# Kernel optimization log

Measured on AMD Instinct MI355X. Metric: run time of the kernel, lower is better.

The kernel has to match this reference:

```python
import jax, jax.numpy as jnp
import numpy as np

B, T, M, H, P, C = 1024, 100, 128, 128, 128, 32  # batch, time, sensors, enc_hid, dec_hid, classes


def setup_inputs() -> dict:
    key = jax.random.key(0)
    ks = jax.random.split(key, 20)
    def n(k, shape, s=0.05):
        return jax.random.normal(k, shape, dtype=jnp.float32) * s
    return {
        "X": n(ks[0], (B, T, M), 1.0),
        # encoder LSTM (input_size=M, hidden=H), PyTorch gate order i,f,g,o
        "enc_Wih": n(ks[1], (4 * H, M)),
        "enc_Whh": n(ks[2], (4 * H, H)),
        "enc_bih": n(ks[3], (4 * H,)),
        "enc_bhh": n(ks[4], (4 * H,)),
        # encoder attention Linear(2H+T -> 1)
        "enc_attn_W": n(ks[5], (1, 2 * H + T)),
        "enc_attn_b": n(ks[6], (1,)),
        # decoder attn: Linear(2P+H -> H), Tanh, Linear(H -> 1)
        "dec_W1": n(ks[7], (H, 2 * P + H)),
        "dec_b1": n(ks[8], (H,)),
        "dec_W2": n(ks[9], (1, H)),
        "dec_b2": n(ks[10], (1,)),
        # decoder LSTM (input_size=1, hidden=P)
        "dec_Wih": n(ks[11], (4 * P, 1)),
        "dec_Whh": n(ks[12], (4 * P, P)),
        "dec_bih": n(ks[13], (4 * P,)),
        "dec_bhh": n(ks[14], (4 * P,)),
        # fc: Linear(H -> 1) with weight.data.normal_() (std 1)
        "fc_W": n(ks[15], (1, H), 1.0),
        "fc_b": n(ks[16], (1,)),
        # fc_final: Linear(P+H -> num_class)
        "fcf_W": n(ks[17], (C, P + H)),
        "fcf_b": n(ks[18], (C,)),
    }


def _lstm_step(x, h, c, Wih, Whh, bih, bhh):
    g = x @ Wih.T + bih + h @ Whh.T + bhh
    i, f, gg, o = jnp.split(g, 4, axis=-1)
    c = jax.nn.sigmoid(f) * c + jax.nn.sigmoid(i) * jnp.tanh(gg)
    h = jax.nn.sigmoid(o) * jnp.tanh(c)
    return h, c


def reference(X, enc_Wih, enc_Whh, enc_bih, enc_bhh, enc_attn_W, enc_attn_b,
              dec_W1, dec_b1, dec_W2, dec_b2,
              dec_Wih, dec_Whh, dec_bih, dec_bhh,
              fc_W, fc_b, fcf_W, fcf_b):
    Bn = X.shape[0]
    XT = jnp.swapaxes(X, 1, 2)  # [B, M, T] constant across encoder steps
    h0 = jnp.zeros((Bn, H), X.dtype)

    def enc_step(carry, x_t):  # x_t: [B, M]
        h, c = carry
        z = jnp.concatenate([
            jnp.broadcast_to(h[:, None, :], (Bn, M, H)),
            jnp.broadcast_to(c[:, None, :], (Bn, M, H)),
            XT,
        ], axis=-1)  # [B, M, 2H+T]
        score = jnp.einsum('bmf,f->bm', z, enc_attn_W[0]) + enc_attn_b[0]
        alpha = jax.nn.softmax(score, axis=1)
        x_tilde = alpha * x_t
        h, c = _lstm_step(x_tilde, h, c, enc_Wih, enc_Whh, enc_bih, enc_bhh)
        return (h, c), h

    _, hs = jax.lax.scan(enc_step, (h0, h0), jnp.swapaxes(X, 0, 1))
    X_enc = jnp.swapaxes(hs, 0, 1)  # [B, T, H]

    d0 = jnp.zeros((Bn, P), X.dtype)
    ctx0 = jnp.zeros((Bn, H), X.dtype)

    def dec_step(carry, _):
        d, c, _ctx = carry
        z = jnp.concatenate([
            jnp.broadcast_to(d[:, None, :], (Bn, T, P)),
            jnp.broadcast_to(c[:, None, :], (Bn, T, P)),
            X_enc,
        ], axis=-1)  # [B, T, 2P+H]
        hid = jnp.tanh(jnp.einsum('btf,hf->bth', z, dec_W1) + dec_b1)
        score = jnp.einsum('bth,h->bt', hid, dec_W2[0]) + dec_b2[0]
        beta = jax.nn.softmax(score, axis=1)
        ctx = jnp.einsum('bt,bth->bh', beta, X_enc)  # [B, H]
        y_tilde = ctx @ fc_W.T + fc_b  # [B, 1]
        d, c = _lstm_step(y_tilde, d, c, dec_Wih, dec_Whh, dec_bih, dec_bhh)
        return (d, c, ctx), None

    (d, c, ctx), _ = jax.lax.scan(dec_step, (d0, d0, ctx0), None, length=T)
    return jnp.concatenate([d, ctx], axis=-1) @ fcf_W.T + fcf_b  # [B, num_class]
```

## Files before the change

kernel.cpp:

```cpp
#include <hip/hip_runtime.h>


typedef unsigned int   u32;
typedef unsigned short u16;

#define T_  100
#define C_  32
#define NT  512
#define BPB 4
#define TS  132
#define QS  (T_ * NT)
#define SP  160

typedef __attribute__((ext_vector_type(2))) __fp16 h16x2;
typedef __attribute__((ext_vector_type(8))) __fp16 h16x8;
typedef __attribute__((ext_vector_type(4))) float  f32x4;

#if __has_builtin(__builtin_amdgcn_fdot2)
#define HAVE_FDOT2 1
#else
#define HAVE_FDOT2 0
#endif

__device__ __forceinline__ u32 pkh2(float a, float b) {
#if __has_builtin(__builtin_amdgcn_cvt_pkrtz)
  h16x2 p = __builtin_amdgcn_cvt_pkrtz(a, b);
  return __builtin_bit_cast(u32, p);
#else
  union { __fp16 h[2]; u32 u; } v;
  v.h[0] = (__fp16)a; v.h[1] = (__fp16)b;
  return v.u;
#endif
}
__device__ __forceinline__ void unph(u32 p, float& lo, float& hi) {
  union { u32 u; __fp16 h[2]; } v; v.u = p;
  lo = (float)v.h[0]; hi = (float)v.h[1];
}
__device__ __forceinline__ u16 f2h(float f) {
  union { __fp16 h; u16 u; } v; v.h = (__fp16)f; return v.u;
}
__device__ __forceinline__ float h2f(u16 u) {
  union { u16 u; __fp16 h; } v; v.u = u; return (float)v.h;
}
__device__ __forceinline__ float dot2h(u32 w, u32 x, float acc) {
#if HAVE_FDOT2
  return __builtin_amdgcn_fdot2(__builtin_bit_cast(h16x2, w),
                                __builtin_bit_cast(h16x2, x),
                                acc, false);
#else
  float a, b, c, d;
  unph(w, a, b); unph(x, c, d);
  return fmaf(a, c, fmaf(b, d, acc));
#endif
}
__device__ __forceinline__ h16x8 pack8(const float* p) {
  float4 v0 = *(const float4*)p;
  float4 v1 = *(const float4*)(p + 4);
  uint4 u;
  u.x = pkh2(v0.x, v0.y); u.y = pkh2(v0.z, v0.w);
  u.z = pkh2(v1.x, v1.y); u.w = pkh2(v1.z, v1.w);
  return __builtin_bit_cast(h16x8, u);
}
__device__ __forceinline__ h16x8 ldb(const u16* p, int off) {
  return __builtin_bit_cast(h16x8, *(const uint4*)(p + off));
}

#if __has_builtin(__builtin_amdgcn_rcpf)
__device__ __forceinline__ float rcpf_(float x){ return __builtin_amdgcn_rcpf(x); }
#else
__device__ __forceinline__ float rcpf_(float x){ return 1.0f / x; }
#endif
__device__ __forceinline__ float sigm(float x){ return rcpf_(1.0f + __expf(-x)); }
__device__ __forceinline__ float tanh_(float x){
  return 1.0f - 2.0f * rcpf_(1.0f + __expf(2.0f * x));
}
__device__ __forceinline__ u32 tanhpk(u32 eu, u32 uu) {
  h16x2 x = __builtin_bit_cast(h16x2, eu) + __builtin_bit_cast(h16x2, uu);
  const h16x2 one  = {(__fp16)1.0f,  (__fp16)1.0f};
#if __has_builtin(__builtin_elementwise_max) && __has_builtin(__builtin_elementwise_min)
  const h16x2 mone = {(__fp16)-1.0f, (__fp16)-1.0f};
  x = __builtin_elementwise_min(one, __builtin_elementwise_max(x, mone));
#else
  {
    float lo, hi; unph(__builtin_bit_cast(u32, x), lo, hi);
    x = (h16x2){(__fp16)fminf(1.f, fmaxf(-1.f, lo)),
                (__fp16)fminf(1.f, fmaxf(-1.f, hi))};
  }
#endif
  h16x2 x2 = x * x;
  const h16x2 c1 = {(__fp16)0.1333333f,  (__fp16)0.1333333f};
  const h16x2 c0 = {(__fp16)-0.3333333f, (__fp16)-0.3333333f};
  h16x2 r = x * (x2 * (x2 * c1 + c0) + one);
  return __builtin_bit_cast(u32, r);
}
__device__ __forceinline__ float ptanh(float x){
  x = fminf(1.0f, fmaxf(-1.0f, x));
  float x2 = x * x;
  float p  = fmaf(x2, 0.1333333f, -0.3333333f);
  return x * fmaf(x2, p, 1.0f);
}
__device__ __forceinline__ float wsum(float v){
  #pragma unroll
  for (int o = 32; o; o >>= 1) v += __shfl_xor(v, o, 64);
  return v;
}

__global__ void __launch_bounds__(NT)
darnn4(const float* __restrict__ X,
       const float* __restrict__ eWih, const float* __restrict__ eWhh,
       const float* __restrict__ ebih, const float* __restrict__ ebhh,
       const float* __restrict__ eAw,  const float* __restrict__ eAb,
       const float* __restrict__ dW1,  const float* __restrict__ db1,
       const float* __restrict__ dW2,  const float* __restrict__ db2,
       const float* __restrict__ dWih, const float* __restrict__ dWhh,
       const float* __restrict__ dbih, const float* __restrict__ dbhh,
       const float* __restrict__ fcW,  const float* __restrict__ fcb,
       const float* __restrict__ fcfW, const float* __restrict__ fcfb,
       u16* __restrict__ qws,
       float* __restrict__ out)
{
  __shared__ __align__(16) u16   sE1[BPB][T_ * TS];
  __shared__ __align__(16) float sg[BPB][520];
  __shared__ __align__(16) float sh[BPB][128];
  __shared__ __align__(16) float sc[BPB][128];
  __shared__ __align__(16) u16   shp[BPB][SP];
  __shared__ __align__(16) u16   scp[BPB][SP];
  __shared__ __align__(16) float su[BPB][128];
  __shared__ __align__(16) float spart[BPB][512];
  __shared__ __align__(16) float sye[BPB][128];
  __shared__ __align__(16) u32   su2[BPB][68];
  __shared__ __align__(16) u32   sw2p[64];
  __shared__ float sred[16];

  const int tid  = threadIdx.x;
  const int lane = tid & 63;
  const int wv   = tid >> 6;
  const int hh   = tid & 127;
  const int q4   = tid >> 7;
  const int nn   = lane & 15;
  const int kg   = lane >> 4;
  const bool wr  = (nn < BPB);
  const int b0   = blockIdx.x * BPB;

  (void)eAb; (void)db2;

  if (tid < 64) sw2p[tid] = pkh2(dW2[2 * tid], dW2[2 * tid + 1]);

  {
    const float* xp = X + (size_t)(b0 + q4) * 12800 + hh;
    float sval = 0.f;
    #pragma unroll 4
    for (int t = 0; t < T_; ++t) sval += xp[t * 128] * eAw[256 + t];
    float e = __expf(sval);
    float s = wsum(e);
    if (lane == 0) sred[wv] = s;
    __syncthreads();
    float al = e * rcpf_(sred[q4 * 2] + sred[q4 * 2 + 1]);
    #pragma unroll 4
    for (int t = 0; t < T_; ++t)
      sE1[q4][t * TS + hh] = f2h(al * xp[t * 128]);
    sh[q4][hh] = 0.f; sc[q4][hh] = 0.f; shp[q4][hh] = 0; scp[q4][hh] = 0;
  }
  __syncthreads();

  {
    u32 wq[64];
    const float4* wi = (const float4*)(eWih + (size_t)tid * 128);
    #pragma unroll
    for (int i = 0; i < 32; ++i) {
      float4 v = wi[i];
      wq[2*i]   = pkh2(v.x, v.y);
      wq[2*i+1] = pkh2(v.z, v.w);
    }
    #pragma unroll 1
    for (int bg = 0; bg < BPB; ++bg) {
      u16* qb = qws + (size_t)(b0 + bg) * QS;
      #pragma unroll 1
      for (int t = 0; t < T_; ++t) {
        const uint2* xr = (const uint2*)(&sE1[bg][t * TS]);
        float a0 = 0.f, a1 = 0.f;
        #pragma unroll
        for (int k = 0; k < 16; ++k) {
          uint2 xv = xr[k];
          a0 = dot2h(wq[2*k],   xv.x, a0);
          a1 = dot2h(wq[2*k+1], xv.y, a1);
        }
        qb[t * NT + tid] = f2h(a0 + a1);
      }
    }
  }
  __syncthreads();

  {
    h16x8 aH[16];
    #pragma unroll
    for (int rt = 0; rt < 4; ++rt)
      #pragma unroll
      for (int ks = 0; ks < 4; ++ks)
        aH[rt*4+ks] = pack8(eWhh + (size_t)(wv*64 + rt*16 + nn) * 128
                            + ks*32 + kg*8);
    float bgx = ebih[hh]       + ebhh[hh];
    float bgy = ebih[hh + 128] + ebhh[hh + 128];
    float bgz = ebih[hh + 256] + ebhh[hh + 256];
    float bgw = ebih[hh + 384] + ebhh[hh + 384];
    const u16* qrow = qws + (size_t)(b0 + q4) * QS + hh;

    for (int t = 0; t < T_; ++t) {
      u16 qv0 = qrow[t * NT];
      u16 qv1 = qrow[t * NT + 128];
      u16 qv2 = qrow[t * NT + 256];
      u16 qv3 = qrow[t * NT + 384];
      f32x4 g0 = {0,0,0,0}, g1 = {0,0,0,0}, g2 = {0,0,0,0}, g3 = {0,0,0,0};
      #pragma unroll
      for (int ks = 0; ks < 4; ++ks) {
        h16x8 b = ldb(&shp[nn & 3][0], ks*32 + kg*8);
        g0 = __builtin_amdgcn_mfma_f32_16x16x32_f16(aH[0*4+ks], b, g0, 0,0,0);
        g1 = __builtin_amdgcn_mfma_f32_16x16x32_f16(aH[1*4+ks], b, g1, 0,0,0);
        g2 = __builtin_amdgcn_mfma_f32_16x16x32_f16(aH[2*4+ks], b, g2, 0,0,0);
        g3 = __builtin_amdgcn_mfma_f32_16x16x32_f16(aH[3*4+ks], b, g3, 0,0,0);
      }
      if (wr) {
        *(f32x4*)(&sg[nn][wv*64 +  0 + kg*4]) = g0;
        *(f32x4*)(&sg[nn][wv*64 + 16 + kg*4]) = g1;
        *(f32x4*)(&sg[nn][wv*64 + 32 + kg*4]) = g2;
        *(f32x4*)(&sg[nn][wv*64 + 48 + kg*4]) = g3;
      }
      __syncthreads();
      {
        float gi = sigm (sg[q4][hh]       + bgx + h2f(qv0));
        float gf = sigm (sg[q4][hh + 128] + bgy + h2f(qv1));
        float gg = tanh_(sg[q4][hh + 256] + bgz + h2f(qv2));
        float go = sigm (sg[q4][hh + 384] + bgw + h2f(qv3));
        float c  = gf * sc[q4][hh] + gi * gg;
        sc[q4][hh] = c;
        float h  = go * tanh_(c);
        sh[q4][hh] = h;
        u16 hb = f2h(h);
        shp[q4][hh] = hb;
        scp[q4][hh] = f2h(c);
        qws[(size_t)(b0 + q4) * QS + t * NT + hh] = hb;
      }
      __syncthreads();
    }
  }

  if (hh < T_) {
    #pragma unroll 1
    for (int bg = 0; bg < BPB; ++bg) {
      const uint2* xe = (const uint2*)(qws + (size_t)(b0 + bg) * QS
                                       + hh * NT + q4 * 32);
      const float* fw = fcW + q4 * 32;
      float a = 0.f;
      #pragma unroll
      for (int k = 0; k < 8; ++k) {
        uint2 xv = xe[k];
        float l0, l1, l2, l3;
        unph(xv.x, l0, l1); unph(xv.y, l2, l3);
        a += fw[4*k]*l0 + fw[4*k+1]*l1 + fw[4*k+2]*l2 + fw[4*k+3]*l3;
      }
      spart[bg][hh * 4 + q4] = a;
    }
  }
  __syncthreads();
  if (hh < T_) {
    float4 p = ((const float4*)spart[q4])[hh];
    sye[q4][hh] = (p.x + p.y) + (p.z + p.w);
  }
  __syncthreads();

  {
    u32 wtp[64];
    const float4* w4p = (const float4*)(dW1 + (size_t)hh * 384 + 256);
    #pragma unroll
    for (int i = 0; i < 32; ++i) {
      float4 v = w4p[i];
      wtp[2*i]   = pkh2(v.x, v.y);
      wtp[2*i+1] = pkh2(v.z, v.w);
    }
    float b1v = db1[hh];
    #pragma unroll 1
    for (int bg = 0; bg < BPB; ++bg) {
      #pragma unroll 1
      for (int i = 0; i < 25; ++i) {
        int t = q4 * 25 + i;
        const uint2* xe = (const uint2*)(qws + (size_t)(b0 + bg) * QS + t * NT);
        float a0 = 0.f, a1 = 0.f;
        #pragma unroll
        for (int k = 0; k < 16; ++k) {
          uint2 xv = xe[k];
          a0 = dot2h(wtp[2*k],   xv.x, a0);
          a1 = dot2h(wtp[2*k+1], xv.y, a1);
        }
        sE1[bg][t * TS + hh] = f2h(a0 + a1 + b1v);
      }
    }
  }

  h16x8 aD[16];
  #pragma unroll
  for (int rt = 0; rt < 4; ++rt)
    #pragma unroll
    for (int ks = 0; ks < 4; ++ks)
      aD[rt*4+ks] = pack8(dWhh + (size_t)(wv*64 + rt*16 + nn) * 128
                          + ks*32 + kg*8);
  h16x8 aU[8];
  #pragma unroll
  for (int ks = 0; ks < 8; ++ks)
    aU[ks] = pack8(dW1 + (size_t)(wv*16 + nn) * 384 + ks*32 + kg*8);
  float bdx = dbih[hh]       + dbhh[hh];
  float bdy = dbih[hh + 128] + dbhh[hh + 128];
  float bdz = dbih[hh + 256] + dbhh[hh + 256];
  float bdw = dbih[hh + 384] + dbhh[hh + 384];
  float wix = dWih[hh];
  float wiy = dWih[hh + 128];
  float wiz = dWih[hh + 256];
  float wiw = dWih[hh + 384];
  float fcbv = fcb[0];
  sh[q4][hh] = 0.f; sc[q4][hh] = 0.f; shp[q4][hh] = 0; scp[q4][hh] = 0;
  __syncthreads();

  for (int step = 0; step < T_; ++step) {
    {
      f32x4 au = {0,0,0,0};
      #pragma unroll
      for (int ks = 0; ks < 8; ++ks) {
        const u16* bp = (ks < 4) ? &shp[nn & 3][0] : &scp[nn & 3][0];
        h16x8 b = ldb(bp, (ks & 3)*32 + kg*8);
        au = __builtin_amdgcn_mfma_f32_16x16x32_f16(aU[ks], b, au, 0,0,0);
      }
      if (wr) {
        uint2 up;
        up.x = pkh2(au[0], au[1]);
        up.y = pkh2(au[2], au[3]);
        *(uint2*)(&su2[nn][wv*8 + kg*2]) = up;
      }
    }
    {
      f32x4 g0 = {0,0,0,0}, g1 = {0,0,0,0}, g2 = {0,0,0,0}, g3 = {0,0,0,0};
      #pragma unroll
      for (int ks = 0; ks < 4; ++ks) {
        h16x8 b = ldb(&shp[nn & 3][0], ks*32 + kg*8);
        g0 = __builtin_amdgcn_mfma_f32_16x16x32_f16(aD[0*4+ks], b, g0, 0,0,0);
        g1 = __builtin_amdgcn_mfma_f32_16x16x32_f16(aD[1*4+ks], b, g1, 0,0,0);
        g2 = __builtin_amdgcn_mfma_f32_16x16x32_f16(aD[2*4+ks], b, g2, 0,0,0);
        g3 = __builtin_amdgcn_mfma_f32_16x16x32_f16(aD[3*4+ks], b, g3, 0,0,0);
      }
      if (wr) {
        *(f32x4*)(&sg[nn][wv*64 +  0 + kg*4]) = g0;
        *(f32x4*)(&sg[nn][wv*64 + 16 + kg*4]) = g1;
        *(f32x4*)(&sg[nn][wv*64 + 32 + kg*4]) = g2;
        *(f32x4*)(&sg[nn][wv*64 + 48 + kg*4]) = g3;
      }
    }
    __syncthreads();
    if (hh < T_) {
      const uint2* wp  = (const uint2*)(sw2p + q4 * 16);
      const uint2* e0p = (const uint2*)(&sE1[0][hh * TS + q4 * 32]);
      const uint2* e1p = (const uint2*)(&sE1[1][hh * TS + q4 * 32]);
      const uint2* e2p = (const uint2*)(&sE1[2][hh * TS + q4 * 32]);
      const uint2* e3p = (const uint2*)(&sE1[3][hh * TS + q4 * 32]);
      const uint2* u0p = (const uint2*)(su2[0] + q4 * 16);
      const uint2* u1p = (const uint2*)(su2[1] + q4 * 16);
      const uint2* u2p = (const uint2*)(su2[2] + q4 * 16);
      const uint2* u3p = (const uint2*)(su2[3] + q4 * 16);
      float ac0 = 0.f, ac1 = 0.f, ac2 = 0.f, ac3 = 0.f;
      #pragma unroll
      for (int j = 0; j < 8; ++j) {
        uint2 w2v = wp[j];
        uint2 ev, uv;
        ev = e0p[j]; uv = u0p[j];
        ac0 = dot2h(w2v.x, tanhpk(ev.x, uv.x), ac0);
        ac0 = dot2h(w2v.y, tanhpk(ev.y, uv.y), ac0);
        ev = e1p[j]; uv = u1p[j];
        ac1 = dot2h(w2v.x, tanhpk(ev.x, uv.x), ac1);
        ac1 = dot2h(w2v.y, tanhpk(ev.y, uv.y), ac1);
        ev = e2p[j]; uv = u2p[j];
        ac2 = dot2h(w2v.x, tanhpk(ev.x, uv.x), ac2);
        ac2 = dot2h(w2v.y, tanhpk(ev.y, uv.y), ac2);
        ev = e3p[j]; uv = u3p[j];
        ac3 = dot2h(w2v.x, tanhpk(ev.x, uv.x), ac3);
        ac3 = dot2h(w2v.y, tanhpk(ev.y, uv.y), ac3);
      }
      spart[0][hh * 4 + q4] = ac0;
      spart[1][hh * 4 + q4] = ac1;
      spart[2][hh * 4 + q4] = ac2;
      spart[3][hh * 4 + q4] = ac3;
    }
    __syncthreads();
    {
      float yv;
      {
        const int bg = q4;
        float4 p0 = ((const float4*)spart[bg])[lane];
        float e0 = __expf((p0.x + p0.y) + (p0.z + p0.w));
        float es = e0, ys = e0 * sye[bg][lane];
        if (lane < 36) {
          float4 p1 = ((const float4*)spart[bg])[64 + lane];
          float e1 = __expf((p1.x + p1.y) + (p1.z + p1.w));
          es += e1; ys += e1 * sye[bg][64 + lane];
        }
        es = wsum(es); ys = wsum(ys);
        yv = ys * rcpf_(es) + fcbv;
      }
      float gi = sigm (sg[q4][hh]       + bdx + wix * yv);
      float gf = sigm (sg[q4][hh + 128] + bdy + wiy * yv);
      float gg = tanh_(sg[q4][hh + 256] + bdz + wiz * yv);
      float go = sigm (sg[q4][hh + 384] + bdw + wiw * yv);
      float c  = gf * sc[q4][hh] + gi * gg;
      sc[q4][hh] = c;
      float d  = go * tanh_(c);
      sh[q4][hh] = d;
      shp[q4][hh] = f2h(d);
      scp[q4][hh] = f2h(c);
    }
    __syncthreads();
  }

  if (wv < BPB) {
    int bg = wv;
    float4 p0 = ((const float4*)spart[bg])[lane];
    float e0 = __expf((p0.x + p0.y) + (p0.z + p0.w));
    float e1 = 0.f;
    if (lane < 36) {
      float4 p1 = ((const float4*)spart[bg])[64 + lane];
      e1 = __expf((p1.x + p1.y) + (p1.z + p1.w));
    }
    float iv = rcpf_(wsum(e0 + e1));
    sye[bg][lane] = e0 * iv;
    if (lane < 36) sye[bg][64 + lane] = e1 * iv;
  }
  __syncthreads();
  {
    const u16* xeb = qws + (size_t)(b0 + q4) * QS + hh;
    float cx = 0.f;
    #pragma unroll 4
    for (int t = 0; t < T_; ++t)
      cx += sye[q4][t] * h2f(xeb[t * NT]);
    su[q4][hh] = cx;
  }
  __syncthreads();
  if (tid < BPB * C_) {
    int bg = tid >> 5, cls = tid & 31;
    const float* w = fcfW + (size_t)cls * 256;
    float acc = fcfb[cls];
    #pragma unroll 8
    for (int k = 0; k < 128; ++k)
      acc += w[k] * sh[bg][k] + w[128 + k] * su[bg][k];
    out[(size_t)(b0 + bg) * C_ + cls] = acc;
  }
}

__global__ void __launch_bounds__(NT)
darnn_fb(const float* __restrict__ X,
         const float* __restrict__ eWih, const float* __restrict__ eWhh,
         const float* __restrict__ ebih, const float* __restrict__ ebhh,
         const float* __restrict__ eAw,
         const float* __restrict__ dW1,  const float* __restrict__ db1,
         const float* __restrict__ dW2,
         const float* __restrict__ dWih, const float* __restrict__ dWhh,
         const float* __restrict__ dbih, const float* __restrict__ dbhh,
         const float* __restrict__ fcW,  const float* __restrict__ fcb,
         const float* __restrict__ fcfW, const float* __restrict__ fcfb,
         float* __restrict__ out)
{
  __shared__ __align__(16) u16   sxh[12800];
  __shared__ __align__(16) u16   sXe[12800];
  __shared__ __align__(16) float sg[512];
  __shared__ __align__(16) float sh[128];
  __shared__ __align__(16) float sc[128];
  __shared__ __align__(16) u16   shp[128];
  __shared__ __align__(16) u16   scp[128];
  __shared__ __align__(16) float su[128];
  __shared__ __align__(16) float spart[512];
  __shared__ __align__(16) float sscore[128];
  __shared__ __align__(16) float sctx[128];
  __shared__ float sred[8];
  __shared__ float sredY[2];

  const int tid  = threadIdx.x;
  const int lane = tid & 63;
  const int wv   = tid >> 6;
  const int b    = blockIdx.x;
  const int hh   = tid & 127;
  const int q4   = tid >> 7;

  {
    const float4* Xb4 = (const float4*)(X + (size_t)b * 12800);
    u32* dst = (u32*)sxh;
    #pragma unroll
    for (int i = 0; i < 7; ++i) {
      int idx = tid + NT * i;
      if (idx < 3200) {
        float4 v = Xb4[idx];
        dst[2*idx]   = pkh2(v.x, v.y);
        dst[2*idx+1] = pkh2(v.z, v.w);
      }
    }
  }
  __syncthreads();
  float sval = 0.f;
  if (tid < 128) {
    #pragma unroll 4
    for (int t = 0; t < T_; ++t)
      sval += h2f(sxh[t * 128 + tid]) * eAw[256 + t];
  }
  float ee = (tid < 128) ? __expf(sval) : 0.f;
  float sm = wsum(ee);
  if (lane == 0 && wv < 2) sred[2 + wv] = sm;
  __syncthreads();
  if (tid < 128) {
    su[tid] = ee * rcpf_(sred[2] + sred[3]);
    sh[tid] = 0.f; sc[tid] = 0.f; shp[tid] = 0; scp[tid] = 0;
  }
  __syncthreads();
  {
    u32* sx32 = (u32*)sxh;
    #pragma unroll
    for (int i = 0; i < 13; ++i) {
      int p = tid + NT * i;
      if (p < 6400) {
        float lo, hi; unph(sx32[p], lo, hi);
        int m = (2 * p) & 127;
        sx32[p] = pkh2(lo * su[m], hi * su[m + 1]);
      }
    }
  }
  __syncthreads();

  u32 wpkH[64], wpkI[64];
  {
    const float4* wr = (const float4*)(eWhh + (size_t)tid * 128);
    #pragma unroll
    for (int i = 0; i < 32; ++i) {
      float4 v = wr[i];
      wpkH[2*i] = pkh2(v.x, v.y); wpkH[2*i+1] = pkh2(v.z, v.w);
    }
    const float4* wi = (const float4*)(eWih + (size_t)tid * 128);
    #pragma unroll
    for (int i = 0; i < 32; ++i) {
      float4 v = wi[i];
      wpkI[2*i] = pkh2(v.x, v.y); wpkI[2*i+1] = pkh2(v.z, v.w);
    }
  }
  float biasg = ebih[tid] + ebhh[tid];

  for (int t = 0; t < T_; ++t) {
    float a0 = biasg, a1 = 0.f, a2 = 0.f, a3 = 0.f;
    const uint4* hr = (const uint4*)(const u32*)shp;
    #pragma unroll
    for (int k = 0; k < 16; ++k) {
      uint4 hv = hr[k];
      a0 = dot2h(wpkH[4*k+0], hv.x, a0);
      a1 = dot2h(wpkH[4*k+1], hv.y, a1);
      a2 = dot2h(wpkH[4*k+2], hv.z, a2);
      a3 = dot2h(wpkH[4*k+3], hv.w, a3);
    }
    const uint4* xr = (const uint4*)((const u32*)sxh + t * 64);
    #pragma unroll
    for (int k = 0; k < 16; ++k) {
      uint4 xv = xr[k];
      a0 = dot2h(wpkI[4*k+0], xv.x, a0);
      a1 = dot2h(wpkI[4*k+1], xv.y, a1);
      a2 = dot2h(wpkI[4*k+2], xv.z, a2);
      a3 = dot2h(wpkI[4*k+3], xv.w, a3);
    }
    sg[tid] = (a0 + a1) + (a2 + a3);
    __syncthreads();
    if (tid < 128) {
      float gi = sigm(sg[tid]);
      float gf = sigm(sg[tid + 128]);
      float gg = tanh_(sg[tid + 256]);
      float go = sigm(sg[tid + 384]);
      float c  = gf * sc[tid] + gi * gg;
      sc[tid]  = c;
      float h  = go * tanh_(c);
      sh[tid]  = h;
      u16 hb = f2h(h);
      shp[tid] = hb; scp[tid] = f2h(c);
      sXe[t * 128 + tid] = hb;
    }
    __syncthreads();
  }

  {
    u32 wtp[64];
    const float4* w4 = (const float4*)(dW1 + (size_t)hh * 384 + 256);
    #pragma unroll
    for (int i = 0; i < 32; ++i) {
      float4 v = w4[i];
      wtp[2*i] = pkh2(v.x, v.y); wtp[2*i+1] = pkh2(v.z, v.w);
    }
    float b1v = db1[hh];
    u16 e1out[25];
    #pragma unroll 1
    for (int i = 0; i < 25; ++i) {
      int t = q4 * 25 + i;
      const uint4* xe4 = (const uint4*)(sXe + t * 128);
      float a0 = 0.f, a1 = 0.f;
      #pragma unroll
      for (int k = 0; k < 16; ++k) {
        uint4 xv = xe4[k];
        a0 = dot2h(wtp[4*k+0], xv.x, a0);
        a1 = dot2h(wtp[4*k+1], xv.y, a1);
        a0 = dot2h(wtp[4*k+2], xv.z, a0);
        a1 = dot2h(wtp[4*k+3], xv.w, a1);
      }
      e1out[i] = f2h(a0 + a1 + b1v);
    }
    __syncthreads();
    #pragma unroll 1
    for (int i = 0; i < 25; ++i)
      sxh[(q4 * 25 + i) * 128 + hh] = e1out[i];
  }

  u32 wpkD[64];
  {
    const float4* wr = (const float4*)(dWhh + (size_t)tid * 128);
    #pragma unroll
    for (int i = 0; i < 32; ++i) {
      float4 v = wr[i];
      wpkD[2*i] = pkh2(v.x, v.y); wpkD[2*i+1] = pkh2(v.z, v.w);
    }
  }
  u32 wtpU[32];
  {
    const float4* wu = (const float4*)(dW1 + (size_t)hh * 384 + q4 * 64);
    #pragma unroll
    for (int i = 0; i < 16; ++i) {
      float4 v = wu[i];
      wtpU[2*i] = pkh2(v.x, v.y); wtpU[2*i+1] = pkh2(v.z, v.w);
    }
  }
  float biasD = dbih[tid] + dbhh[tid];
  float wihj  = dWih[tid];
  float w2a   = dW2[lane];
  float w2b   = dW2[lane + 64];
  float fcbv  = fcb[0];
  float fcwv  = (tid < 128) ? fcW[tid] : 0.f;
  if (tid < 128) { sh[tid] = 0.f; sc[tid] = 0.f; shp[tid] = 0; scp[tid] = 0; }
  __syncthreads();

  for (int step = 0; step < T_; ++step) {
    {
      const u32* base = (q4 < 2) ? (const u32*)shp : (const u32*)scp;
      const uint4* vp = (const uint4*)(base + (q4 & 1) * 32);
      float a0 = 0.f, a1 = 0.f;
      #pragma unroll
      for (int k = 0; k < 8; ++k) {
        uint4 v = vp[k];
        a0 = dot2h(wtpU[4*k+0], v.x, a0);
        a1 = dot2h(wtpU[4*k+1], v.y, a1);
        a0 = dot2h(wtpU[4*k+2], v.z, a0);
        a1 = dot2h(wtpU[4*k+3], v.w, a1);
      }
      spart[q4 * 128 + hh] = a0 + a1;
    }
    __syncthreads();
    {
      float ul = spart[lane] + spart[128 + lane]
               + spart[256 + lane] + spart[384 + lane];
      float uh = spart[64 + lane] + spart[192 + lane]
               + spart[320 + lane] + spart[448 + lane];
      #pragma unroll 1
      for (int i = 0; i < 13; ++i) {
        int t = wv + 8 * i;
        if (t < T_) {
          float v = w2a * ptanh(h2f(sxh[t * 128 + lane]) + ul)
                  + w2b * ptanh(h2f(sxh[t * 128 + 64 + lane]) + uh);
          v = wsum(v);
          if (lane == 0) sscore[t] = v;
        }
      }
    }
    __syncthreads();
    if (wv == 0) {
      float s0 = sscore[lane];
      float E0 = __expf(s0);
      float E1v = (lane < 36) ? __expf(sscore[lane + 64]) : 0.f;
      float s  = wsum(E0 + E1v);
      float iv = rcpf_(s);
      sscore[lane] = E0 * iv;
      if (lane < 36) sscore[lane + 64] = E1v * iv;
    }
    __syncthreads();
    {
      float pc = 0.f;
      #pragma unroll
      for (int i = 0; i < 25; ++i) {
        int t = q4 * 25 + i;
        pc += sscore[t] * h2f(sXe[t * 128 + hh]);
      }
      spart[q4 * 128 + hh] = pc;
    }
    __syncthreads();
    {
      float v = 0.f;
      if (tid < 128) {
        float cx = spart[tid] + spart[tid + 128]
                 + spart[tid + 256] + spart[tid + 384];
        sctx[tid] = cx;
        v = fcwv * cx;
      }
      v = wsum(v);
      if (lane == 0 && wv < 2) sredY[wv] = v;
    }
    __syncthreads();
    {
      float yt = sredY[0] + sredY[1] + fcbv;
      float a0 = biasD + wihj * yt, a1 = 0.f, a2 = 0.f, a3 = 0.f;
      const uint4* hr = (const uint4*)(const u32*)shp;
      #pragma unroll
      for (int k = 0; k < 16; ++k) {
        uint4 hv = hr[k];
        a0 = dot2h(wpkD[4*k+0], hv.x, a0);
        a1 = dot2h(wpkD[4*k+1], hv.y, a1);
        a2 = dot2h(wpkD[4*k+2], hv.z, a2);
        a3 = dot2h(wpkD[4*k+3], hv.w, a3);
      }
      sg[tid] = (a0 + a1) + (a2 + a3);
    }
    __syncthreads();
    if (tid < 128) {
      float gi = sigm(sg[tid]);
      float gf = sigm(sg[tid + 128]);
      float gg = tanh_(sg[tid + 256]);
      float go = sigm(sg[tid + 384]);
      float c  = gf * sc[tid] + gi * gg;
      sc[tid]  = c;
      float d  = go * tanh_(c);
      sh[tid]  = d;
      shp[tid] = f2h(d);
      scp[tid] = f2h(c);
    }
    __syncthreads();
  }

  if (tid < C_) {
    float acc = fcfb[tid];
    const float* w = fcfW + (size_t)tid * 256;
    #pragma unroll 8
    for (int k = 0; k < 128; ++k)
      acc += w[k] * sh[k] + w[128 + k] * sctx[k];
    out[(size_t)b * C_ + tid] = acc;
  }
}

extern "C" void kernel_launch(void* const* d_in, const int* in_sizes, int n_in,
                              void* d_out, int out_size, void* d_ws, size_t ws_size,
                              hipStream_t stream) {
  (void)n_in; (void)out_size;
  const float* X    = (const float*)d_in[0];
  const float* eWih = (const float*)d_in[1];
  const float* eWhh = (const float*)d_in[2];
  const float* ebih = (const float*)d_in[3];
  const float* ebhh = (const float*)d_in[4];
  const float* eAw  = (const float*)d_in[5];
  const float* eAb  = (const float*)d_in[6];
  const float* dW1  = (const float*)d_in[7];
  const float* db1  = (const float*)d_in[8];
  const float* dW2  = (const float*)d_in[9];
  const float* db2  = (const float*)d_in[10];
  const float* dWih = (const float*)d_in[11];
  const float* dWhh = (const float*)d_in[12];
  const float* dbih = (const float*)d_in[13];
  const float* dbhh = (const float*)d_in[14];
  const float* fcW  = (const float*)d_in[15];
  const float* fcb  = (const float*)d_in[16];
  const float* fcfW = (const float*)d_in[17];
  const float* fcfb = (const float*)d_in[18];
  float* out = (float*)d_out;

  const int B = in_sizes[0] / (T_ * 128);
  const size_t needQ = (size_t)B * QS * sizeof(u16);
  if (ws_size >= needQ && (B % BPB) == 0) {
    darnn4<<<dim3(B / BPB), dim3(NT), 0, stream>>>(
        X, eWih, eWhh, ebih, ebhh, eAw, eAb,
        dW1, db1, dW2, db2, dWih, dWhh, dbih, dbhh,
        fcW, fcb, fcfW, fcfb, (u16*)d_ws, out);
  } else {
    darnn_fb<<<dim3(B), dim3(NT), 0, stream>>>(
        X, eWih, eWhh, ebih, ebhh, eAw,
        dW1, db1, dW2, dWih, dWhh, dbih, dbhh,
        fcW, fcb, fcfW, fcfb, out);
  }
}
```

Baseline: 734.2 us.

## Move encoder input projection and decoder E1 precompute to MFMA, overlap gate MFMA

```diff
diff --git a/kernel.cpp b/kernel.cpp
--- a/kernel.cpp
+++ b/kernel.cpp
@@ -105,7 +105,7 @@
   return v;
 }
 
-__global__ void __launch_bounds__(NT)
+__global__ void __launch_bounds__(NT, 1)
 darnn4(const float* __restrict__ X,
        const float* __restrict__ eWih, const float* __restrict__ eWhh,
        const float* __restrict__ ebih, const float* __restrict__ ebhh,
@@ -140,6 +140,8 @@
   const int nn   = lane & 15;
   const int kg   = lane >> 4;
   const bool wr  = (nn < BPB);
+  const int tq   = nn >> 2;
+  const int bq   = nn & 3;
   const int b0   = blockIdx.x * BPB;
 
   (void)eAb; (void)db2;
@@ -164,29 +166,32 @@
   __syncthreads();
 
   {
-    u32 wq[64];
-    const float4* wi = (const float4*)(eWih + (size_t)tid * 128);
-    #pragma unroll
-    for (int i = 0; i < 32; ++i) {
-      float4 v = wi[i];
-      wq[2*i]   = pkh2(v.x, v.y);
-      wq[2*i+1] = pkh2(v.z, v.w);
-    }
+    h16x8 aQ[16];
+    #pragma unroll
+    for (int mt = 0; mt < 4; ++mt)
+      #pragma unroll
+      for (int ks = 0; ks < 4; ++ks)
+        aQ[mt*4+ks] = pack8(eWih + (size_t)(wv*64 + mt*16 + nn) * 128
+                            + ks*32 + kg*8);
     #pragma unroll 1
-    for (int bg = 0; bg < BPB; ++bg) {
-      u16* qb = qws + (size_t)(b0 + bg) * QS;
-      #pragma unroll 1
-      for (int t = 0; t < T_; ++t) {
-        const uint2* xr = (const uint2*)(&sE1[bg][t * TS]);
-        float a0 = 0.f, a1 = 0.f;
-        #pragma unroll
-        for (int k = 0; k < 16; ++k) {
-          uint2 xv = xr[k];
-          a0 = dot2h(wq[2*k],   xv.x, a0);
-          a1 = dot2h(wq[2*k+1], xv.y, a1);
-        }
-        qb[t * NT + tid] = f2h(a0 + a1);
-      }
+    for (int tn = 0; tn < 25; ++tn) {
+      const int t = tn * 4 + tq;
+      const u16* xb = &sE1[bq][t * TS];
+      f32x4 c0={0,0,0,0}, c1={0,0,0,0}, c2={0,0,0,0}, c3={0,0,0,0};
+      #pragma unroll
+      for (int ks = 0; ks < 4; ++ks) {
+        h16x8 b = ldb(xb, ks*32 + kg*8);
+        c0 = __builtin_amdgcn_mfma_f32_16x16x32_f16(aQ[0*4+ks], b, c0, 0,0,0);
+        c1 = __builtin_amdgcn_mfma_f32_16x16x32_f16(aQ[1*4+ks], b, c1, 0,0,0);
+        c2 = __builtin_amdgcn_mfma_f32_16x16x32_f16(aQ[2*4+ks], b, c2, 0,0,0);
+        c3 = __builtin_amdgcn_mfma_f32_16x16x32_f16(aQ[3*4+ks], b, c3, 0,0,0);
+      }
+      u16* qb = qws + (size_t)(b0 + bq) * QS + (size_t)t * NT + wv*64 + kg*4;
+      uint2 p;
+      p.x = pkh2(c0[0], c0[1]); p.y = pkh2(c0[2], c0[3]); *(uint2*)(qb)      = p;
+      p.x = pkh2(c1[0], c1[1]); p.y = pkh2(c1[2], c1[3]); *(uint2*)(qb + 16) = p;
+      p.x = pkh2(c2[0], c2[1]); p.y = pkh2(c2[2], c2[3]); *(uint2*)(qb + 32) = p;
+      p.x = pkh2(c3[0], c3[1]); p.y = pkh2(c3[2], c3[3]); *(uint2*)(qb + 48) = p;
     }
   }
   __syncthreads();
@@ -269,30 +274,25 @@
   __syncthreads();
 
   {
-    u32 wtp[64];
-    const float4* w4p = (const float4*)(dW1 + (size_t)hh * 384 + 256);
-    #pragma unroll
-    for (int i = 0; i < 32; ++i) {
-      float4 v = w4p[i];
-      wtp[2*i]   = pkh2(v.x, v.y);
-      wtp[2*i+1] = pkh2(v.z, v.w);
-    }
-    float b1v = db1[hh];
+    h16x8 aE[4];
+    #pragma unroll
+    for (int ks = 0; ks < 4; ++ks)
+      aE[ks] = pack8(dW1 + (size_t)(wv*16 + nn) * 384 + 256 + ks*32 + kg*8);
+    float4 b1 = *(const float4*)(db1 + wv*16 + kg*4);
     #pragma unroll 1
-    for (int bg = 0; bg < BPB; ++bg) {
-      #pragma unroll 1
-      for (int i = 0; i < 25; ++i) {
-        int t = q4 * 25 + i;
-        const uint2* xe = (const uint2*)(qws + (size_t)(b0 + bg) * QS + t * NT);
-        float a0 = 0.f, a1 = 0.f;
-        #pragma unroll
-        for (int k = 0; k < 16; ++k) {
-          uint2 xv = xe[k];
-          a0 = dot2h(wtp[2*k],   xv.x, a0);
-          a1 = dot2h(wtp[2*k+1], xv.y, a1);
-        }
-        sE1[bg][t * TS + hh] = f2h(a0 + a1 + b1v);
-      }
+    for (int tn = 0; tn < 25; ++tn) {
+      const int t = tn * 4 + tq;
+      const u16* xb = qws + (size_t)(b0 + bq) * QS + (size_t)t * NT;
+      f32x4 c = {0,0,0,0};
+      #pragma unroll
+      for (int ks = 0; ks < 4; ++ks) {
+        h16x8 b = ldb(xb, ks*32 + kg*8);
+        c = __builtin_amdgcn_mfma_f32_16x16x32_f16(aE[ks], b, c, 0,0,0);
+      }
+      uint2 p;
+      p.x = pkh2(c[0] + b1.x, c[1] + b1.y);
+      p.y = pkh2(c[2] + b1.z, c[3] + b1.w);
+      *(uint2*)(&sE1[bq][t * TS + wv*16 + kg*4]) = p;
     }
   }
 
@@ -335,24 +335,16 @@
         *(uint2*)(&su2[nn][wv*8 + kg*2]) = up;
       }
     }
-    {
-      f32x4 g0 = {0,0,0,0}, g1 = {0,0,0,0}, g2 = {0,0,0,0}, g3 = {0,0,0,0};
-      #pragma unroll
-      for (int ks = 0; ks < 4; ++ks) {
-        h16x8 b = ldb(&shp[nn & 3][0], ks*32 + kg*8);
-        g0 = __builtin_amdgcn_mfma_f32_16x16x32_f16(aD[0*4+ks], b, g0, 0,0,0);
-        g1 = __builtin_amdgcn_mfma_f32_16x16x32_f16(aD[1*4+ks], b, g1, 0,0,0);
-        g2 = __builtin_amdgcn_mfma_f32_16x16x32_f16(aD[2*4+ks], b, g2, 0,0,0);
-        g3 = __builtin_amdgcn_mfma_f32_16x16x32_f16(aD[3*4+ks], b, g3, 0,0,0);
-      }
-      if (wr) {
-        *(f32x4*)(&sg[nn][wv*64 +  0 + kg*4]) = g0;
-        *(f32x4*)(&sg[nn][wv*64 + 16 + kg*4]) = g1;
-        *(f32x4*)(&sg[nn][wv*64 + 32 + kg*4]) = g2;
-        *(f32x4*)(&sg[nn][wv*64 + 48 + kg*4]) = g3;
-      }
-    }
-    __syncthreads();
+    __syncthreads();
+    f32x4 g0 = {0,0,0,0}, g1 = {0,0,0,0}, g2 = {0,0,0,0}, g3 = {0,0,0,0};
+    #pragma unroll
+    for (int ks = 0; ks < 4; ++ks) {
+      h16x8 b = ldb(&shp[nn & 3][0], ks*32 + kg*8);
+      g0 = __builtin_amdgcn_mfma_f32_16x16x32_f16(aD[0*4+ks], b, g0, 0,0,0);
+      g1 = __builtin_amdgcn_mfma_f32_16x16x32_f16(aD[1*4+ks], b, g1, 0,0,0);
+      g2 = __builtin_amdgcn_mfma_f32_16x16x32_f16(aD[2*4+ks], b, g2, 0,0,0);
+      g3 = __builtin_amdgcn_mfma_f32_16x16x32_f16(aD[3*4+ks], b, g3, 0,0,0);
+    }
     if (hh < T_) {
       const uint2* wp  = (const uint2*)(sw2p + q4 * 16);
       const uint2* e0p = (const uint2*)(&sE1[0][hh * TS + q4 * 32]);
@@ -385,6 +377,12 @@
       spart[1][hh * 4 + q4] = ac1;
       spart[2][hh * 4 + q4] = ac2;
       spart[3][hh * 4 + q4] = ac3;
+    }
+    if (wr) {
+      *(f32x4*)(&sg[nn][wv*64 +  0 + kg*4]) = g0;
+      *(f32x4*)(&sg[nn][wv*64 + 16 + kg*4]) = g1;
+      *(f32x4*)(&sg[nn][wv*64 + 32 + kg*4]) = g2;
+      *(f32x4*)(&sg[nn][wv*64 + 48 + kg*4]) = g3;
     }
     __syncthreads();
     {
```

After: 648.5 us. 1.13x faster.
